# Kernel optimization log

Hardware: AMD Instinct MI355X
Metric: run time of the kernel (lower is better)

Reference implementation:

```python
import jax, jax.numpy as jnp
import numpy as np

ITERS = 4
LN_EPS = 1e-5


def build_grid(H, W):
    # standard uORF grid in [-1, 1], shape (H, W, 2), last dim = (x, y)
    x = jnp.linspace(-1.0 + 1.0 / W, 1.0 - 1.0 / W, W)
    y = jnp.linspace(-1.0 + 1.0 / H, 1.0 - 1.0 / H, H)
    yy, xx = jnp.meshgrid(y, x, indexing='ij')
    return jnp.stack([xx, yy], axis=-1)


def ln(x, g, b):
    m = jnp.mean(x, axis=-1, keepdims=True)
    v = jnp.var(x, axis=-1, keepdims=True)
    return (x - m) * jax.lax.rsqrt(v + LN_EPS) * g + b


def setup_inputs():
    key = jax.random.key(0)
    ks = jax.random.split(key, 16)
    B, H, W, C, K, Ds = 4, 64, 64, 256, 5, 256
    s = 0.02
    inp = {
        'feat': jax.random.normal(ks[0], (B, H, W, C), jnp.float32),
        'mask': (jax.random.uniform(ks[1], (K, 1, H, W)) > 0.5).astype(jnp.float32),
        'noise': jax.random.normal(ks[2], (B, K, Ds), jnp.float32),
        'slots_mu': jax.random.normal(ks[3], (1, 1, Ds), jnp.float32),
        'slots_logsigma': jax.random.normal(ks[4], (1, 1, Ds), jnp.float32) * s,
        'norm_g': jnp.ones((C,), jnp.float32), 'norm_b': jnp.zeros((C,), jnp.float32),
        'grid_W': jax.random.normal(ks[5], (C, 4), jnp.float32) * s,
        'grid_b': jnp.zeros((C,), jnp.float32),
        'k_W': jax.random.normal(ks[6], (C, C), jnp.float32) * s,
        'v_W': jax.random.normal(ks[7], (C, C), jnp.float32) * s,
        'mlp_g': jnp.ones((C,), jnp.float32), 'mlp_b': jnp.zeros((C,), jnp.float32),
        'mlp_W': jax.random.normal(ks[8], (Ds, C), jnp.float32) * s,
        'mlp_bias': jnp.zeros((Ds,), jnp.float32),
        'q_g': jnp.ones((Ds,), jnp.float32), 'q_b': jnp.zeros((Ds,), jnp.float32),
        'q_W': jax.random.normal(ks[9], (Ds, Ds), jnp.float32) * s,
        'gru_Wih': jax.random.normal(ks[10], (3 * Ds, Ds), jnp.float32) * s,
        'gru_Whh': jax.random.normal(ks[11], (3 * Ds, Ds), jnp.float32) * s,
        'gru_bih': jnp.zeros((3 * Ds,), jnp.float32),
        'gru_bhh': jnp.zeros((3 * Ds,), jnp.float32),
        'res_g': jnp.ones((Ds,), jnp.float32), 'res_b': jnp.zeros((Ds,), jnp.float32),
        'res_W': jax.random.normal(ks[12], (Ds, Ds), jnp.float32) * s,
        'res_bias': jnp.zeros((Ds,), jnp.float32),
    }
    return inp


def reference(feat, mask, noise, slots_mu, slots_logsigma, norm_g, norm_b,
              grid_W, grid_b, k_W, v_W, mlp_g, mlp_b, mlp_W, mlp_bias,
              q_g, q_b, q_W, gru_Wih, gru_Whh, gru_bih, gru_bhh,
              res_g, res_b, res_W, res_bias):
    B, H, W, C = feat.shape
    K = mask.shape[0]
    N = H * W
    Ds = slots_mu.shape[-1]
    scale = Ds ** -0.5

    grid = build_grid(H, W)                                   # (H, W, 2)
    # foreground positions: mask-weighted mean of grid -> (K, 2)
    g = jnp.transpose(grid, (2, 0, 1))[None]                  # (1, 2, H, W)
    fg_pos = jnp.sum(g * mask, axis=(2, 3)) / (jnp.sum(mask, axis=(2, 3)) + 1e-5)
    fg_pos = jnp.broadcast_to(fg_pos[None], (B, K, 2))        # (B, K, 2)

    feat_n = ln(feat.reshape(B, N, C), norm_g, norm_b)        # (B, N, C)
    mask_flat = mask.reshape(K, N)
    slot = slots_mu + jnp.exp(slots_logsigma) * noise         # (B, K, Ds)

    # k, v with relative position embedding; fg_pos never changes in-loop,
    # so compute once (the original recomputes the same values each iter).
    rel = grid.reshape(1, 1, N, 2) - fg_pos[:, :, None, :]    # (B, K, N, 2)
    rel4 = jnp.concatenate([rel, -rel], axis=-1)              # (B, K, N, 4)
    ge = rel4 @ grid_W.T + grid_b                             # (B, K, N, C)
    kbase = feat_n @ k_W.T                                    # (B, N, C)
    vbase = feat_n @ v_W.T
    kk = ln(kbase[:, None] + ge, mlp_g, mlp_b) @ mlp_W.T + mlp_bias  # (B,K,N,Ds)
    vv = ln(vbase[:, None] + ge, mlp_g, mlp_b) @ mlp_W.T + mlp_bias

    attn_vis = None
    for _ in range(ITERS):
        slot_prev = slot
        q = ln(slot, q_g, q_b) @ q_W.T                        # (B, K, Ds)
        attn = jnp.einsum('bkd,bknd->bkn', q, kk) * scale
        attn = jnp.where(mask_flat[None] == 0, -1e9, attn)
        attn = jax.nn.softmax(attn, axis=-1)                  # (B, K, N)
        upd = jnp.einsum('bkn,bknd->bkd', attn, vv)           # (B, K, Ds)
        # torch GRUCell
        x = upd.reshape(-1, Ds)
        h = slot.reshape(-1, Ds)
        gi = x @ gru_Wih.T + gru_bih
        gh = h @ gru_Whh.T + gru_bhh
        ir, iz, inn = jnp.split(gi, 3, axis=-1)
        hr, hz, hn = jnp.split(gh, 3, axis=-1)
        r = jax.nn.sigmoid(ir + hr)
        z = jax.nn.sigmoid(iz + hz)
        n = jnp.tanh(inn + r * hn)
        hnew = ((1.0 - z) * n + z * h).reshape(B, K, Ds)
        slot = (ln(hnew, res_g, res_b) @ res_W.T + res_bias) + slot_prev
        amin = attn.min(axis=-1, keepdims=True)
        amax = attn.max(axis=-1, keepdims=True)
        attn_vis = (attn - amin) / (amax - amin + 1e-5)
    return slot, fg_pos, attn_vis
```

## Files before the change

kernel.cpp:

```cpp
#include <hip/hip_runtime.h>
#include <math.h>

typedef unsigned short u16;
typedef unsigned int   u32;
typedef short bf8v __attribute__((ext_vector_type(8)));
typedef float f4v  __attribute__((ext_vector_type(4)));

static constexpr int B_=4, C_=256, K_=5, D_=256, N_=4096, IT_=4;
static constexpr float EPS_=1e-5f;
static constexpr int P0_MISC=96, P0_UQ=97, P0_FG=98, P0_GRID=103;
static constexpr int BT_QP=256, BT_TR=276, BT_GRID=404;

__device__ __forceinline__ float bf2f(u16 u){ u32 x=((u32)u)<<16; float f; __builtin_memcpy(&f,&x,4); return f; }
__device__ __forceinline__ float bflo(u32 u){ u32 x=u<<16; float f; __builtin_memcpy(&f,&x,4); return f; }
__device__ __forceinline__ float bfhi(u32 u){ u32 x=u&0xffff0000u; float f; __builtin_memcpy(&f,&x,4); return f; }
__device__ __forceinline__ u16 f2bf(float f){ u32 x; __builtin_memcpy(&x,&f,4); u32 r=x+0x7fffu+((x>>16)&1u); return (u16)(r>>16); }
__device__ __forceinline__ float ldin(const void* p, size_t i, int f){
  return f ? ((const float*)p)[i] : bf2f(((const u16*)p)[i]);
}
__device__ __forceinline__ void stout(void* p, size_t i, float v, int f){
  if (f) ((float*)p)[i]=v; else ((u16*)p)[i]=f2bf(v);
}
__device__ __forceinline__ int sw16(int row,int col){
  return row*256 + ((((col>>3)^(row&7))<<3) | (col&7));
}

__device__ __forceinline__ void breduce4(float&a,float&b,float&c,float&d,float* red){
  #pragma unroll
  for(int o=32;o>0;o>>=1){
    a+=__shfl_down(a,o,64); b+=__shfl_down(b,o,64);
    c+=__shfl_down(c,o,64); d+=__shfl_down(d,o,64);
  }
  int w=threadIdx.x>>6;
  __syncthreads();
  if((threadIdx.x&63)==0){ red[w]=a; red[4+w]=b; red[8+w]=c; red[12+w]=d; }
  __syncthreads();
  a=red[0]+red[1]+red[2]+red[3];
  b=red[4]+red[5]+red[6]+red[7];
  c=red[8]+red[9]+red[10]+red[11];
  d=red[12]+red[13]+red[14]+red[15];
}
__device__ __forceinline__ void breduce4_16(float&a,float&b,float&c,float&d,float* red){
  #pragma unroll
  for(int o=32;o>0;o>>=1){
    a+=__shfl_down(a,o,64); b+=__shfl_down(b,o,64);
    c+=__shfl_down(c,o,64); d+=__shfl_down(d,o,64);
  }
  int w=threadIdx.x>>6;
  __syncthreads();
  if((threadIdx.x&63)==0){ red[w]=a; red[16+w]=b; red[32+w]=c; red[48+w]=d; }
  __syncthreads();
  a=0;b=0;c=0;d=0;
  #pragma unroll
  for(int i=0;i<16;++i){ a+=red[i]; b+=red[16+i]; c+=red[32+i]; d+=red[48+i]; }
}

__device__ __forceinline__ int probe_f(const void* feat, float* red){
  const u32* p=(const u32*)feat;
  int t=threadIdx.x; int bad=0;
  #pragma unroll
  for(int s=0;s<8;++s){
    u32 wd=p[t+s*256];
    float lo=bf2f((u16)(wd&0xffffu));
    if(!(fabsf(lo)<1e6f)) bad++;
  }
  float bb=(float)bad, z1=0,z2=0,z3=0;
  breduce4(bb,z1,z2,z3,red);
  return (bb>=16.f)?1:0;
}

__global__ void prep0_kernel(const void* feat,
    const void* kW, const void* vW, const void* mW,
    const void* mu, const void* lsig, const void* noise,
    const void* gW, const void* gb_, const void* mg,
    const void* mb_, const void* mbias, const void* mask,
    int* flag, float* slot, float* gvec,
    u16* Wkb, u16* Wvb, u16* Wgb,
    float* Uvec, float* Qs, float* fg, void* out)
{
  __shared__ float redp[16];
  int bid=blockIdx.x;
  int t=threadIdx.x;
  int f=probe_f(feat, redp);
  if(bid==0 && t==0) *flag=f;
  __syncthreads();
  if(bid<P0_MISC){
    int which=bid>>5;
    int base=(bid&31)*2048;
    if(which==0){
      #pragma unroll
      for(int s=0;s<8;++s){ int e=base+s*256+t; Wkb[e]=f2bf(ldin(kW,e,f)); }
    } else if(which==1){
      #pragma unroll
      for(int s=0;s<8;++s){ int e=base+s*256+t; Wvb[e]=f2bf(ldin(vW,e,f)); }
    } else {
      #pragma unroll
      for(int s=0;s<8;++s){ int e=base+s*256+t; int c=e&255; Wgb[e]=f2bf(ldin(mg,c,f)*ldin(mW,e,f)); }
    }
    return;
  }
  if(bid==P0_MISC){
    #pragma unroll
    for(int s=0;s<20;++s){ int e=s*256+t; int d=e&255;
      slot[e]=ldin(mu,d,f)+expf(ldin(lsig,d,f))*ldin(noise,e,f); }
    #pragma unroll
    for(int s=0;s<3;++s){ int e=s*256+t;
      int c=e&255, sel=e>>8;
      float v;
      if(sel==0)      v=ldin(gW,c*4+0,f)-ldin(gW,c*4+2,f);
      else if(sel==1) v=ldin(gW,c*4+1,f)-ldin(gW,c*4+3,f);
      else            v=ldin(gb_,c,f);
      gvec[e]=v;
    }
    return;
  }
  __shared__ float s_a[256], s_b[256], s_c[256];
  if(bid==P0_UQ){
    __shared__ float s_mg[256], s_mb[256];
    s_a[t]=ldin(gW,t*4+0,f)-ldin(gW,t*4+2,f);
    s_b[t]=ldin(gW,t*4+1,f)-ldin(gW,t*4+3,f);
    s_c[t]=ldin(gb_,t,f);
    s_mg[t]=ldin(mg,t,f);
    s_mb[t]=ldin(mb_,t,f);
    __syncthreads();
    float u1=0,u2=0,u3=0,gw=0,bw=0;
    if(f){
      const float4* rp=(const float4*)mW + (size_t)t*64;
      #pragma unroll 8
      for(int j=0;j<64;++j){
        float4 v4=rp[j]; int c=j*4;
        float m0=v4.x,m1=v4.y,m2=v4.z,m3=v4.w;
        float w0=s_mg[c]*m0, w1=s_mg[c+1]*m1, w2=s_mg[c+2]*m2, w3=s_mg[c+3]*m3;
        u1+=s_a[c]*w0+s_a[c+1]*w1+s_a[c+2]*w2+s_a[c+3]*w3;
        u2+=s_b[c]*w0+s_b[c+1]*w1+s_b[c+2]*w2+s_b[c+3]*w3;
        u3+=s_c[c]*w0+s_c[c+1]*w1+s_c[c+2]*w2+s_c[c+3]*w3;
        gw+=w0+w1+w2+w3;
        bw+=s_mb[c]*m0+s_mb[c+1]*m1+s_mb[c+2]*m2+s_mb[c+3]*m3;
      }
    } else {
      const bf8v* rp=(const bf8v*)((const u16*)mW + (size_t)t*256);
      #pragma unroll 8
      for(int j=0;j<32;++j){
        bf8v v8=rp[j]; int c=j*8;
        #pragma unroll
        for(int e=0;e<8;++e){
          float mwv=bf2f((u16)(unsigned short)v8[e]);
          float wg=s_mg[c+e]*mwv;
          u1+=s_a[c+e]*wg; u2+=s_b[c+e]*wg; u3+=s_c[c+e]*wg; gw+=wg;
          bw+=s_mb[c+e]*mwv;
        }
      }
    }
    Uvec[t]=u1; Uvec[256+t]=u2; Uvec[512+t]=u3; Uvec[768+t]=gw;
    Uvec[1024+t]=bw+ldin(mbias,t,f);
    float a=s_a[t], b=s_b[t], cc=s_c[t];
    float s0=a*a,s1=b*b,s2=cc*cc,s3=a*b; breduce4(s0,s1,s2,s3,redp);
    float s4=a*cc,s5=b*cc,s6=a,s7=b;     breduce4(s4,s5,s6,s7,redp);
    float s8=cc,z1=0,z2=0,z3=0;          breduce4(s8,z1,z2,z3,redp);
    if(t==0){
      Qs[0]=s0; Qs[1]=s1; Qs[2]=s2; Qs[3]=s3; Qs[4]=s4; Qs[5]=s5;
      Qs[6]=s6*(1.f/256.f); Qs[7]=s7*(1.f/256.f); Qs[8]=s8*(1.f/256.f);
    }
  } else {
    int k=bid-P0_FG;
    float sx=0,sy=0,sm=0;
    #pragma unroll
    for(int s=0;s<16;++s){
      int p=t+s*256;
      float m=ldin(mask,(size_t)k*N_+p,f);
      int i=p>>6, j=p&63;
      float x=(2*j+1)*(1.0f/64.0f)-1.0f;
      float y=(2*i+1)*(1.0f/64.0f)-1.0f;
      sx+=x*m; sy+=y*m; sm+=m;
    }
    float d=0;
    breduce4(sx,sy,sm,d,redp);
    if(t==0){
      float inv=1.0f/(sm+1e-5f);
      float fx=sx*inv, fy=sy*inv;
      fg[k*2]=fx; fg[k*2+1]=fy;
      for(int b=0;b<B_;++b){
        stout(out, 5120+(b*K_+k)*2+0, fx, f);
        stout(out, 5120+(b*K_+k)*2+1, fy, f);
      }
    }
  }
}

__global__ void __launch_bounds__(512,2) base_kernel(const int* flag, const void* feat, const void* ng, const void* nb,
    const u16* Wkb, const u16* Wvb, const u16* Wgb, const float* gvec,
    float* scal, u16* PkT, u16* Pvb,
    const float* slot, const void* qg, const void* qb_, const void* qW,
    const void* rW, const void* Wih, const void* Whh,
    float* WqT, float* WrT, float* WihT, float* WhhT,
    float* qbuf)
{
  extern __shared__ u16 smem[];
  u16* bufA = smem;
  u16* bufB = smem + 16384;
  int t=threadIdx.x, f=*flag;
  if(blockIdx.x>=BT_TR){
    float (*tile)[65] = (float(*)[65])smem;
    int b2=blockIdx.x-BT_TR;
    const void* src; float* dst; int OS;
    if(b2<16){ src=qW; dst=WqT; OS=256; }
    else if(b2<32){ src=rW; dst=WrT; OS=256; b2-=16; }
    else if(b2<80){ src=Wih; dst=WihT; OS=768; b2-=32; }
    else { src=Whh; dst=WhhT; OS=768; b2-=80; }
    int r0=(b2>>2)*64, c0=(b2&3)*64;
    int lane=t&63, wv=t>>6;
    #pragma unroll
    for(int it=0;it<8;++it){
      int i=wv*8+it;
      tile[i][lane]=ldin(src,(size_t)(r0+i)*256+c0+lane,f);
    }
    __syncthreads();
    #pragma unroll
    for(int it=0;it<8;++it){
      int i=wv*8+it;
      dst[(size_t)(c0+i)*OS + r0 + lane] = tile[lane][i];
    }
    return;
  }
  if(blockIdx.x>=BT_QP){
    float* Lq =(float*)smem;
    float* pp =(float*)smem+256;
    float* red=(float*)smem+768;
    int bk=blockIdx.x-BT_QP;
    int tt=t&255, hh=t>>8, w=t>>6;
    float x=slot[bk*256+tt];
    float s=x, s2=x*x;
    #pragma unroll
    for(int o=32;o>0;o>>=1){ s+=__shfl_down(s,o,64); s2+=__shfl_down(s2,o,64); }
    if((t&63)==0){ red[w]=s; red[8+w]=s2; }
    __syncthreads();
    s=0; s2=0;
    #pragma unroll
    for(int i=0;i<8;++i){ s+=red[i]; s2+=red[8+i]; }
    float m=s*(1.f/512.f), v=s2*(1.f/512.f)-m*m;
    float lq=(x-m)*rsqrtf(v+EPS_)*ldin(qg,tt,f)+ldin(qb_,tt,f);
    if(hh==0) Lq[tt]=lq;
    __syncthreads();
    float acc=0; int cb=hh*128;
    if(f){
      const float4* rp=(const float4*)qW + ((size_t)tt*256+cb)/4;
      #pragma unroll 8
      for(int j=0;j<32;++j){
        float4 v4=rp[j]; int c=cb+j*4;
        acc+=Lq[c]*v4.x+Lq[c+1]*v4.y+Lq[c+2]*v4.z+Lq[c+3]*v4.w;
      }
    } else {
      const bf8v* rp=(const bf8v*)((const u16*)qW + (size_t)tt*256+cb);
      #pragma unroll 8
      for(int j=0;j<16;++j){
        bf8v v8=rp[j]; int c=cb+j*8;
        #pragma unroll
        for(int e=0;e<8;++e) acc+=Lq[c+e]*bf2f((u16)(unsigned short)v8[e]);
      }
    }
    pp[hh*256+tt]=acc;
    __syncthreads();
    if(hh==0) qbuf[bk*256+tt]=pp[tt]+pp[256+tt];
    return;
  }
  int w=t>>6, l=t&63;
  int quad=l>>4, m=l&15;
  int row0=blockIdx.x*64;
  {
    float g0=ldin(ng,4*l+0,f), g1=ldin(ng,4*l+1,f), g2=ldin(ng,4*l+2,f), g3=ldin(ng,4*l+3,f);
    float b0=ldin(nb,4*l+0,f), b1=ldin(nb,4*l+1,f), b2=ldin(nb,4*l+2,f), b3=ldin(nb,4*l+3,f);
    #pragma unroll
    for(int r8=0;r8<8;++r8){
      int row=8*w+r8;
      float x0,x1,x2,x3;
      if(f){
        float4 v4=((const float4*)feat)[(size_t)(row0+row)*64+l];
        x0=v4.x; x1=v4.y; x2=v4.z; x3=v4.w;
      } else {
        ushort4 uu=((const ushort4*)feat)[(size_t)(row0+row)*64+l];
        x0=bf2f(uu.x); x1=bf2f(uu.y); x2=bf2f(uu.z); x3=bf2f(uu.w);
      }
      float s=x0+x1+x2+x3, s2=x0*x0+x1*x1+x2*x2+x3*x3;
      #pragma unroll
      for(int o=32;o>0;o>>=1){ s+=__shfl_xor(s,o,64); s2+=__shfl_xor(s2,o,64); }
      float mm=s*(1.f/256.f), inv=rsqrtf(s2*(1.f/256.f)-mm*mm+EPS_);
      ushort4 o4=make_ushort4(f2bf((x0-mm)*inv*g0+b0), f2bf((x1-mm)*inv*g1+b1),
                              f2bf((x2-mm)*inv*g2+b2), f2bf((x3-mm)*inv*g3+b3));
      *(ushort4*)&bufA[sw16(row,4*l)]=o4;
    }
  }
  __syncthreads();
  {
    f4v ack[4][2], acv[4][2];
    #pragma unroll
    for(int rt=0;rt<4;++rt)
      #pragma unroll
      for(int i=0;i<2;++i){ ack[rt][i]=(f4v){0.f,0.f,0.f,0.f}; acv[rt][i]=(f4v){0.f,0.f,0.f,0.f}; }
    #pragma unroll
    for(int kk=0;kk<8;++kk){
      int kcol=kk*32+quad*8;
      bf8v af[4];
      #pragma unroll
      for(int rt=0;rt<4;++rt) af[rt]=*(bf8v*)&bufA[sw16(rt*16+m,kcol)];
      #pragma unroll
      for(int i=0;i<2;++i){
        int n=w*32+16*i+m;
        bf8v bk=*(const bf8v*)(Wkb+(size_t)n*256+kcol);
        bf8v bv=*(const bf8v*)(Wvb+(size_t)n*256+kcol);
        #pragma unroll
        for(int rt=0;rt<4;++rt){
          ack[rt][i]=__builtin_amdgcn_mfma_f32_16x16x32_bf16(af[rt],bk,ack[rt][i],0,0,0);
          acv[rt][i]=__builtin_amdgcn_mfma_f32_16x16x32_bf16(af[rt],bv,acv[rt][i],0,0,0);
        }
      }
    }
    #pragma unroll
    for(int rt=0;rt<4;++rt)
      #pragma unroll
      for(int i=0;i<2;++i){
        int n=w*32+16*i+m;
        #pragma unroll
        for(int r=0;r<4;++r)
          bufB[sw16(rt*16+quad*4+r,n)]=f2bf(ack[rt][i][r]);
      }
    __syncthreads();
    #pragma unroll
    for(int rt=0;rt<4;++rt)
      #pragma unroll
      for(int i=0;i<2;++i){
        int n=w*32+16*i+m;
        #pragma unroll
        for(int r=0;r<4;++r)
          bufA[sw16(rt*16+quad*4+r,n)]=f2bf(acv[rt][i][r]);
      }
  }
  __syncthreads();
  {
    float gA0=gvec[l], gA1=gvec[l+64], gA2=gvec[l+128], gA3=gvec[l+192];
    float gB0=gvec[256+l], gB1=gvec[256+l+64], gB2=gvec[256+l+128], gB3=gvec[256+l+192];
    float gC0=gvec[512+l], gC1=gvec[512+l+64], gC2=gvec[512+l+128], gC3=gvec[512+l+192];
    for(int r8=0;r8<8;++r8){
      int row=8*w+r8;
      float k0=bf2f(bufB[sw16(row,l)]),     k1=bf2f(bufB[sw16(row,l+64)]),
            k2=bf2f(bufB[sw16(row,l+128)]), k3=bf2f(bufB[sw16(row,l+192)]);
      float x0=bf2f(bufA[sw16(row,l)]),     x1=bf2f(bufA[sw16(row,l+64)]),
            x2=bf2f(bufA[sw16(row,l+128)]), x3=bf2f(bufA[sw16(row,l+192)]);
      float v0=k0+k1+k2+k3;
      float v1=k0*k0+k1*k1+k2*k2+k3*k3;
      float v2=k0*gA0+k1*gA1+k2*gA2+k3*gA3;
      float v3=k0*gB0+k1*gB1+k2*gB2+k3*gB3;
      float v4=k0*gC0+k1*gC1+k2*gC2+k3*gC3;
      float v5=x0+x1+x2+x3;
      float v6=x0*x0+x1*x1+x2*x2+x3*x3;
      float v7=x0*gA0+x1*gA1+x2*gA2+x3*gA3;
      float v8=x0*gB0+x1*gB1+x2*gB2+x3*gB3;
      float v9=x0*gC0+x1*gC1+x2*gC2+x3*gC3;
      #pragma unroll
      for(int o=32;o>0;o>>=1){
        v0+=__shfl_down(v0,o,64); v1+=__shfl_down(v1,o,64); v2+=__shfl_down(v2,o,64);
        v3+=__shfl_down(v3,o,64); v4+=__shfl_down(v4,o,64); v5+=__shfl_down(v5,o,64);
        v6+=__shfl_down(v6,o,64); v7+=__shfl_down(v7,o,64); v8+=__shfl_down(v8,o,64);
        v9+=__shfl_down(v9,o,64);
      }
      if(l==0){
        float* sc=scal+(size_t)(row0+row)*10;
        sc[0]=v0; sc[1]=v1; sc[2]=v2; sc[3]=v3; sc[4]=v4;
        sc[5]=v5; sc[6]=v6; sc[7]=v7; sc[8]=v8; sc[9]=v9;
      }
    }
  }
  {
    f4v apk[4][2], apv[4][2];
    #pragma unroll
    for(int rt=0;rt<4;++rt)
      #pragma unroll
      for(int i=0;i<2;++i){ apk[rt][i]=(f4v){0.f,0.f,0.f,0.f}; apv[rt][i]=(f4v){0.f,0.f,0.f,0.f}; }
    #pragma unroll
    for(int kk=0;kk<8;++kk){
      int kcol=kk*32+quad*8;
      bf8v afk[4], afv[4];
      #pragma unroll
      for(int rt=0;rt<4;++rt){
        afk[rt]=*(bf8v*)&bufB[sw16(rt*16+m,kcol)];
        afv[rt]=*(bf8v*)&bufA[sw16(rt*16+m,kcol)];
      }
      #pragma unroll
      for(int i=0;i<2;++i){
        int n=w*32+16*i+m;
        bf8v bg=*(const bf8v*)(Wgb+(size_t)n*256+kcol);
        #pragma unroll
        for(int rt=0;rt<4;++rt){
          apk[rt][i]=__builtin_amdgcn_mfma_f32_16x16x32_bf16(afk[rt],bg,apk[rt][i],0,0,0);
          apv[rt][i]=__builtin_amdgcn_mfma_f32_16x16x32_bf16(afv[rt],bg,apv[rt][i],0,0,0);
        }
      }
    }
    #pragma unroll
    for(int rt=0;rt<4;++rt)
      #pragma unroll
      for(int i=0;i<2;++i){
        int d=w*32+16*i+m;
        *(ushort4*)(PkT+(size_t)d*16384+row0+rt*16+quad*4)=
          make_ushort4(f2bf(apk[rt][i][0]),f2bf(apk[rt][i][1]),f2bf(apk[rt][i][2]),f2bf(apk[rt][i][3]));
      }
    __syncthreads();
    #pragma unroll
    for(int rt=0;rt<4;++rt)
      #pragma unroll
      for(int i=0;i<2;++i){
        int d=w*32+16*i+m;
        #pragma unroll
        for(int r=0;r<4;++r)
          bufB[sw16(rt*16+quad*4+r,d)]=f2bf(apv[rt][i][r]);
      }
  }
  __syncthreads();
  #pragma unroll
  for(int r8=0;r8<8;++r8){
    int row=8*w+r8;
    ushort4 s4=*(ushort4*)&bufB[sw16(row,4*l)];
    *(ushort4*)(Pvb+(size_t)(row0+row)*256+4*l)=s4;
  }
}

__global__ void __launch_bounds__(512) attn_kernel(const int* flag, const float* qbuf, const u16* PkT,
    const float* scal, const float* Qs, const float* Uvec, const float* fg, const void* mask,
    const u16* Pvb, float* logits, float* pmax, float* psum, float* updpart, float* sscp,
    int store_lg)
{
  __shared__ float q5[1280];
  __shared__ float un[10240];
  __shared__ float lgs[320], ivs[320], mvs[320];
  __shared__ float qs5[40], fgs[10], Qss[9], MSl[5];
  __shared__ float sred[8][5][4];
  int tid=threadIdx.x, f=*flag;
  int b=blockIdx.x>>6, ch=blockIdx.x&63;
  int w=tid>>6, l=tid&63;
  int n0=ch<<6;
  for(int p=tid;p<1280;p+=512) q5[p]=qbuf[(size_t)b*1280+p];
  if(tid<10) fgs[tid]=fg[tid];
  if(tid<9)  Qss[tid]=Qs[tid];
  __syncthreads();
  for(int p=w;p<25;p+=8){
    int k=p/5, j=p%5;
    float s=q5[k*256+l]*Uvec[j*256+l]+q5[k*256+l+64]*Uvec[j*256+l+64]
           +q5[k*256+l+128]*Uvec[j*256+l+128]+q5[k*256+l+192]*Uvec[j*256+l+192];
    #pragma unroll
    for(int o=32;o>0;o>>=1) s+=__shfl_xor(s,o,64);
    if(l==0) qs5[k*8+j]=s;
  }
  {
    int n=n0+l; size_t row=(size_t)b*N_+n;
    float dk0=0,dk1=0,dk2=0,dk3=0,dk4=0;
    int cbase=w*32;
    #pragma unroll 8
    for(int cc=0;cc<32;++cc){
      int c=cbase+cc;
      float pv=bf2f(PkT[(size_t)c*16384+row]);
      dk0+=pv*q5[c]; dk1+=pv*q5[256+c]; dk2+=pv*q5[512+c];
      dk3+=pv*q5[768+c]; dk4+=pv*q5[1024+c];
    }
    un[(w*5+0)*64+l]=dk0; un[(w*5+1)*64+l]=dk1; un[(w*5+2)*64+l]=dk2;
    un[(w*5+3)*64+l]=dk3; un[(w*5+4)*64+l]=dk4;
  }
  __syncthreads();
  if(tid<320){
    int k=tid>>6, nl=tid&63;
    float dot=0;
    #pragma unroll
    for(int j=0;j<8;++j) dot+=un[(j*5+k)*64+nl];
    int n2=n0+nl; size_t row2=(size_t)b*N_+n2;
    const float* sc=scal+row2*10;
    float rx=(2*(n2&63)+1)*(1.f/64.f)-1.f-fgs[2*k];
    float ry=(2*(n2>>6)+1)*(1.f/64.f)-1.f-fgs[2*k+1];
    float qge=rx*rx*Qss[0]+ry*ry*Qss[1]+Qss[2]+2.f*(rx*ry*Qss[3]+rx*Qss[4]+ry*Qss[5]);
    float mk=sc[0]*(1.f/256.f)+rx*Qss[6]+ry*Qss[7]+Qss[8];
    float sxk=sc[1]+2.f*(rx*sc[2]+ry*sc[3]+sc[4])+qge;
    float invK=rsqrtf(sxk*(1.f/256.f)-mk*mk+EPS_);
    float lg=invK*(dot+rx*qs5[k*8+0]+ry*qs5[k*8+1]+qs5[k*8+2]-mk*qs5[k*8+3])+qs5[k*8+4];
    float mval=ldin(mask,(size_t)k*N_+n2,f);
    lg=(mval==0.f)? -1e9f : lg*0.0625f;
    if(store_lg) logits[((size_t)(b*5+k))*N_+n2]=lg;
    lgs[tid]=lg;
    float mv=sc[5]*(1.f/256.f)+rx*Qss[6]+ry*Qss[7]+Qss[8];
    float sxv=sc[6]+2.f*(rx*sc[7]+ry*sc[8]+sc[9])+qge;
    mvs[tid]=mv;
    ivs[tid]=rsqrtf(sxv*(1.f/256.f)-mv*mv+EPS_);
  }
  __syncthreads();
  if(tid<64){
    #pragma unroll
    for(int k=0;k<5;++k){
      float v=lgs[k*64+tid];
      float M=v;
      #pragma unroll
      for(int o=32;o>0;o>>=1) M=fmaxf(M,__shfl_xor(M,o,64));
      float e=expf(v-M);
      #pragma unroll
      for(int o=32;o>0;o>>=1) e+=__shfl_xor(e,o,64);
      if(tid==0){ pmax[((size_t)(b*64+ch))*5+k]=M; psum[((size_t)(b*64+ch))*5+k]=e; MSl[k]=M; }
    }
  }
  __syncthreads();
  {
    float acc[5][4]={{0}};
    float swx[5]={0,0,0,0,0}, swy[5]={0,0,0,0,0}, sw[5]={0,0,0,0,0}, swm[5]={0,0,0,0,0};
    #pragma unroll 2
    for(int rr=0;rr<8;++rr){
      int nl=w*8+rr; int n2=n0+nl;
      size_t row=(size_t)b*N_+n2;
      uint2 pu=*(const uint2*)(Pvb+row*256+l*4);
      float px=bflo(pu.x), py=bfhi(pu.x), pz=bflo(pu.y), pw=bfhi(pu.y);
      int jx=n2&63, iy=n2>>6;
      #pragma unroll
      for(int k=0;k<5;++k){
        float wgt=expf(lgs[k*64+nl]-MSl[k])*ivs[k*64+nl];
        float rx=(2*jx+1)*(1.f/64.f)-1.f-fgs[2*k];
        float ry=(2*iy+1)*(1.f/64.f)-1.f-fgs[2*k+1];
        acc[k][0]+=wgt*px; acc[k][1]+=wgt*py; acc[k][2]+=wgt*pz; acc[k][3]+=wgt*pw;
        sw[k]+=wgt; swx[k]+=wgt*rx; swy[k]+=wgt*ry; swm[k]+=wgt*mvs[k*64+nl];
      }
    }
    #pragma unroll
    for(int k=0;k<5;++k)
      *(float4*)&un[(w*5+k)*256+l*4]=make_float4(acc[k][0],acc[k][1],acc[k][2],acc[k][3]);
    if(l==0){
      #pragma unroll
      for(int k=0;k<5;++k){ sred[w][k][0]=swx[k]; sred[w][k][1]=swy[k];
                            sred[w][k][2]=sw[k];  sred[w][k][3]=swm[k]; }
    }
  }
  __syncthreads();
  for(int p=tid;p<1280;p+=512){
    int k=p>>8, d=p&255;
    float v=0;
    #pragma unroll
    for(int j=0;j<8;++j) v+=un[(j*5+k)*256+d];
    updpart[((size_t)blockIdx.x*5+k)*256+d]=v;
  }
  if(tid<20){
    int kk=tid>>2, j=tid&3;
    float s=0;
    #pragma unroll
    for(int jj=0;jj<8;++jj) s+=sred[jj][kk][j];
    sscp[((size_t)blockIdx.x*5+kk)*4+j]=s;
  }
}

__global__ void __launch_bounds__(1024) gru_kernel(const int* flag, float* slot, const float* updpart,
    const float* sscp, const float* Uvec, const float* pmax, const float* psum, const float* logits,
    const float* WihT, const float* WhhT, const void* bih, const void* bhh,
    const void* rg, const void* rb_, const float* WrT, const void* rbias,
    const void* qg, const void* qb_, const float* WqT, float* qbuf,
    int do_vis, void* out)
{
  __shared__ float u[256], h[256], sn[256];
  __shared__ float part[4][6][256];
  __shared__ float red[64];
  __shared__ float cvec[4];
  __shared__ float fch[64];
  __shared__ float MSg[2];
  int tid=threadIdx.x, t=tid&255, g=tid>>8;
  int blk=blockIdx.x;
  int f=*flag;
  if(blk>=20){
    if(!do_vis) return;
    int bk2=blk-20, k2=bk2%K_, b2=bk2/K_;
    if(tid<64){
      float pm=pmax[((size_t)(b2*64+tid))*5+k2];
      float ps=psum[((size_t)(b2*64+tid))*5+k2];
      float M=pm;
      #pragma unroll
      for(int o=32;o>0;o>>=1) M=fmaxf(M,__shfl_xor(M,o,64));
      float e=ps*expf(pm-M);
      #pragma unroll
      for(int o=32;o>0;o>>=1) e+=__shfl_xor(e,o,64);
      if(tid==0){ MSg[0]=M; MSg[1]=1.0f/e; }
    }
    __syncthreads();
    float M=MSg[0], Sinv=MSg[1];
    float a[4]; float mn=1e30f, mx=-1e30f;
    #pragma unroll
    for(int s=0;s<4;++s){
      a[s]=expf(logits[(size_t)bk2*N_+tid+s*1024]-M)*Sinv;
      mn=fminf(mn,a[s]); mx=fmaxf(mx,a[s]);
    }
    #pragma unroll
    for(int o=32;o>0;o>>=1){ mn=fminf(mn,__shfl_down(mn,o,64)); mx=fmaxf(mx,__shfl_down(mx,o,64)); }
    int wv=tid>>6;
    __syncthreads();
    if((tid&63)==0){ red[wv]=mn; red[16+wv]=mx; }
    __syncthreads();
    mn=1e30f; mx=-1e30f;
    #pragma unroll
    for(int i=0;i<16;++i){ mn=fminf(mn,red[i]); mx=fmaxf(mx,red[16+i]); }
    float inv=1.0f/(mx-mn+1e-5f);
    #pragma unroll
    for(int s=0;s<4;++s) stout(out, 5160+(size_t)bk2*N_+tid+s*1024, (a[s]-mn)*inv, f);
    return;
  }
  int bk=blk, k=bk%K_, b=bk/K_;
  if(tid<64){
    float pm=pmax[((size_t)(b*64+tid))*5+k];
    float ps=psum[((size_t)(b*64+tid))*5+k];
    float M=pm;
    #pragma unroll
    for(int o=32;o>0;o>>=1) M=fmaxf(M,__shfl_xor(M,o,64));
    float fc=expf(pm-M);
    fch[tid]=fc;
    float e=ps*fc;
    #pragma unroll
    for(int o=32;o>0;o>>=1) e+=__shfl_xor(e,o,64);
    if(tid==0){ MSg[0]=M; MSg[1]=1.0f/e; }
  }
  __syncthreads();
  float Sinv=MSg[1];
  float ua=0;
  {
    int ch0=g*16;
    #pragma unroll 4
    for(int ci=0;ci<16;++ci){ int ch=ch0+ci; ua += fch[ch]*updpart[(((size_t)(b*64+ch))*5+k)*256+t]; }
  }
  part[g][0][t]=ua;
  if(t<4){
    float s=0;
    #pragma unroll 4
    for(int ci=0;ci<16;++ci){ int ch=g*16+ci; s += fch[ch]*sscp[(((size_t)(b*64+ch))*5+k)*4+t]; }
    part[g][1][t]=s;
  }
  __syncthreads();
  if(g==0 && t<4) cvec[t]=part[0][1][t]+part[1][1][t]+part[2][1][t]+part[3][1][t];
  __syncthreads();
  if(g==0){
    float uu=part[0][0][t]+part[1][0][t]+part[2][0][t]+part[3][0][t];
    u[t]=(uu+cvec[0]*Uvec[t]+cvec[1]*Uvec[256+t]+cvec[2]*Uvec[512+t]-cvec[3]*Uvec[768+t])*Sinv
         +Uvec[1024+t];
    h[t]=slot[bk*256+t];
  }
  __syncthreads();
  float p0=0,p1=0,p2=0,p3=0,p4=0,p5=0;
  int c0=g*64;
  #pragma unroll 8
  for(int cc=0;cc<64;++cc){
    int c=c0+cc;
    float uc=u[c], hc=h[c];
    const float* wi=WihT+(size_t)c*768+t;
    const float* wh=WhhT+(size_t)c*768+t;
    p0+=uc*wi[0]; p1+=uc*wi[256]; p2+=uc*wi[512];
    p3+=hc*wh[0]; p4+=hc*wh[256]; p5+=hc*wh[512];
  }
  part[g][0][t]=p0; part[g][1][t]=p1; part[g][2][t]=p2;
  part[g][3][t]=p3; part[g][4][t]=p4; part[g][5][t]=p5;
  __syncthreads();
  float hn=0;
  if(g==0){
    float gi0=ldin(bih,t,f)+part[0][0][t]+part[1][0][t]+part[2][0][t]+part[3][0][t];
    float gi1=ldin(bih,256+t,f)+part[0][1][t]+part[1][1][t]+part[2][1][t]+part[3][1][t];
    float gi2=ldin(bih,512+t,f)+part[0][2][t]+part[1][2][t]+part[2][2][t]+part[3][2][t];
    float gh0=ldin(bhh,t,f)+part[0][3][t]+part[1][3][t]+part[2][3][t]+part[3][3][t];
    float gh1=ldin(bhh,256+t,f)+part[0][4][t]+part[1][4][t]+part[2][4][t]+part[3][4][t];
    float gh2=ldin(bhh,512+t,f)+part[0][5][t]+part[1][5][t]+part[2][5][t]+part[3][5][t];
    float r=1.f/(1.f+expf(-(gi0+gh0)));
    float z=1.f/(1.f+expf(-(gi1+gh1)));
    float nn=tanhf(gi2+r*gh2);
    hn=(1.f-z)*nn+z*h[t];
  }
  float s=hn, sq=hn*hn, za=0, zb=0;
  breduce4_16(s,sq,za,zb,red);
  if(g==0){
    float m=s*(1.f/256.f), var=sq*(1.f/256.f)-m*m;
    u[t]=(hn-m)*rsqrtf(var+EPS_)*ldin(rg,t,f)+ldin(rb_,t,f);
  }
  __syncthreads();
  float pr=0;
  #pragma unroll 8
  for(int cc=0;cc<64;++cc){ int c=c0+cc; pr+=u[c]*WrT[(size_t)c*256+t]; }
  part[g][0][t]=pr;
  __syncthreads();
  if(g==0){
    float acc=ldin(rbias,t,f)+h[t]+part[0][0][t]+part[1][0][t]+part[2][0][t]+part[3][0][t];
    slot[bk*256+t]=acc;
    stout(out, (size_t)bk*256+t, acc, f);
    sn[t]=acc;
  }
  __syncthreads();
  float xs=(g==0)? sn[t]:0.f;
  float xq=xs*xs, zc=0, zd=0;
  breduce4_16(xs,xq,zc,zd,red);
  if(g==0){
    float m=xs*(1.f/256.f), var=xq*(1.f/256.f)-m*m;
    u[t]=(sn[t]-m)*rsqrtf(var+EPS_)*ldin(qg,t,f)+ldin(qb_,t,f);
  }
  __syncthreads();
  float pq=0;
  #pragma unroll 8
  for(int cc=0;cc<64;++cc){ int c=c0+cc; pq+=u[c]*WqT[(size_t)c*256+t]; }
  part[g][0][t]=pq;
  __syncthreads();
  if(g==0){
    float qv=part[0][0][t]+part[1][0][t]+part[2][0][t]+part[3][0][t];
    qbuf[bk*256+t]=qv;
  }
}

extern "C" void kernel_launch(void* const* d_in, const int* in_sizes, int n_in,
                              void* d_out, int out_size, void* d_ws, size_t ws_size,
                              hipStream_t stream)
{
  const void* feat =d_in[0];  const void* mask =d_in[1];  const void* noise=d_in[2];
  const void* mu   =d_in[3];  const void* lsig =d_in[4];  const void* ng   =d_in[5];
  const void* nb   =d_in[6];  const void* gW   =d_in[7];  const void* gb_  =d_in[8];
  const void* kW   =d_in[9];  const void* vW   =d_in[10]; const void* mg   =d_in[11];
  const void* mb_  =d_in[12]; const void* mW   =d_in[13]; const void* mbias=d_in[14];
  const void* qg   =d_in[15]; const void* qb_  =d_in[16]; const void* qW   =d_in[17];
  const void* Wih  =d_in[18]; const void* Whh  =d_in[19]; const void* bih  =d_in[20];
  const void* bhh  =d_in[21]; const void* rg   =d_in[22]; const void* rb_  =d_in[23];
  const void* rW   =d_in[24]; const void* rbias=d_in[25];

  char* p=(char*)d_ws;
  auto alloc=[&](size_t bytes)->char*{ char* r=p; p+=(bytes+255)&~(size_t)255; return r; };
  int*   flag   =(int*)  alloc(256);
  float* fg     =(float*)alloc(64);
  float* slot   =(float*)alloc(5120*4);
  float* qbuf   =(float*)alloc(5120*4);
  float* logits =(float*)alloc((size_t)81920*4);
  float* pmax   =(float*)alloc(1280*4);
  float* psum   =(float*)alloc(1280*4);
  float* updpart=(float*)alloc((size_t)256*5*256*4);
  float* sscp   =(float*)alloc((size_t)256*5*4*4);
  float* WqT    =(float*)alloc((size_t)65536*4);
  float* WrT    =(float*)alloc((size_t)65536*4);
  float* WihT   =(float*)alloc((size_t)196608*4);
  float* WhhT   =(float*)alloc((size_t)196608*4);
  float* gvec   =(float*)alloc(768*4);
  float* Uvec   =(float*)alloc(1280*4);
  float* Qs     =(float*)alloc(64);
  float* scal   =(float*)alloc((size_t)163840*4);
  u16*   Wkb    =(u16*)  alloc((size_t)65536*2);
  u16*   Wvb    =(u16*)  alloc((size_t)65536*2);
  u16*   Wgb    =(u16*)  alloc((size_t)65536*2);
  u16*   PkT    =(u16*)  alloc((size_t)16384*256*2);
  u16*   Pvb    =(u16*)  alloc((size_t)16384*256*2);

  prep0_kernel<<<P0_GRID,256,0,stream>>>(feat,kW,vW,mW,mu,lsig,noise,gW,gb_,mg,
                                         mb_,mbias,mask,
                                         flag,slot,gvec,Wkb,Wvb,Wgb,
                                         Uvec,Qs,fg,d_out);
  base_kernel<<<BT_GRID,512,65536,stream>>>(flag,feat,ng,nb,Wkb,Wvb,Wgb,gvec,scal,PkT,Pvb,
                                            slot,qg,qb_,qW,rW,Wih,Whh,
                                            WqT,WrT,WihT,WhhT,qbuf);
  for(int it=0; it<IT_; ++it){
    attn_kernel<<<B_*64,512,0,stream>>>(flag,qbuf,PkT,scal,Qs,Uvec,fg,mask,Pvb,
                                        logits,pmax,psum,updpart,sscp,(it==IT_-1)?1:0);
    int nb_g = (it==IT_-1)? 40 : 20;
    gru_kernel<<<nb_g,1024,0,stream>>>(flag,slot,updpart,sscp,Uvec,pmax,psum,logits,
                                       WihT,WhhT,bih,bhh,rg,rb_,WrT,rbias,
                                       qg,qb_,WqT,qbuf,(it==IT_-1)?1:0,d_out);
  }
}
```

Measured before the change: 345.8 us.

## Fuse attention and GRU per iteration using per-batch atomic grid barrier

Merges the attention and GRU kernels into one launch per iteration. Blocks bump a per-batch atomic counter after writing their partials, and designated blocks spin until all 64 blocks of that batch arrive before running the GRU or visualization step. This removes one kernel launch and its gap per iteration. The spin-wait relies on all blocks being co-resident, which risks deadlock, and the larger 1024-thread blocks leave half the threads idle during the attention phase.

```diff
diff --git a/kernel.cpp b/kernel.cpp
--- a/kernel.cpp
+++ b/kernel.cpp
@@ -74,7 +74,7 @@
     const void* mu, const void* lsig, const void* noise,
     const void* gW, const void* gb_, const void* mg,
     const void* mb_, const void* mbias, const void* mask,
-    int* flag, float* slot, float* gvec,
+    int* flag, int* cnt, float* slot, float* gvec,
     u16* Wkb, u16* Wvb, u16* Wgb,
     float* Uvec, float* Qs, float* fg, void* out)
 {
@@ -100,6 +100,7 @@
     return;
   }
   if(bid==P0_MISC){
+    if(t<16) cnt[t]=0;
     #pragma unroll
     for(int s=0;s<20;++s){ int e=s*256+t; int d=e&255;
       slot[e]=ldin(mu,d,f)+expf(ldin(lsig,d,f))*ldin(noise,e,f); }
@@ -423,33 +424,45 @@
   }
 }
 
-__global__ void __launch_bounds__(512) attn_kernel(const int* flag, const float* qbuf, const u16* PkT,
+__global__ void __launch_bounds__(1024,1) iter_kernel(
+    const int* flag, float* qbuf, const u16* PkT,
     const float* scal, const float* Qs, const float* Uvec, const float* fg, const void* mask,
     const u16* Pvb, float* logits, float* pmax, float* psum, float* updpart, float* sscp,
-    int store_lg)
+    int* cntb, int store_lg, int do_vis,
+    float* slot, const float* WihT, const float* WhhT, const void* bih, const void* bhh,
+    const void* rg, const void* rb_, const float* WrT, const void* rbias,
+    const void* qg, const void* qb_, const float* WqT, void* out)
 {
-  __shared__ float q5[1280];
-  __shared__ float un[10240];
-  __shared__ float lgs[320], ivs[320], mvs[320];
-  __shared__ float qs5[40], fgs[10], Qss[9], MSl[5];
-  __shared__ float sred[8][5][4];
+  extern __shared__ float sm[];
+  float* q5  = sm;
+  float* un  = sm+1280;
+  float* lgs = sm+11520;
+  float* ivs = sm+11840;
+  float* mvs = sm+12160;
+  float* qs5 = sm+12480;
+  float* fgs = sm+12520;
+  float* Qss = sm+12530;
+  float* MSl = sm+12539;
+  float* sredf=sm+12544;
   int tid=threadIdx.x, f=*flag;
   int b=blockIdx.x>>6, ch=blockIdx.x&63;
   int w=tid>>6, l=tid&63;
   int n0=ch<<6;
-  for(int p=tid;p<1280;p+=512) q5[p]=qbuf[(size_t)b*1280+p];
+  for(int p=tid;p<1280;p+=1024) q5[p]=qbuf[(size_t)b*1280+p];
   if(tid<10) fgs[tid]=fg[tid];
   if(tid<9)  Qss[tid]=Qs[tid];
   __syncthreads();
-  for(int p=w;p<25;p+=8){
-    int k=p/5, j=p%5;
-    float s=q5[k*256+l]*Uvec[j*256+l]+q5[k*256+l+64]*Uvec[j*256+l+64]
-           +q5[k*256+l+128]*Uvec[j*256+l+128]+q5[k*256+l+192]*Uvec[j*256+l+192];
-    #pragma unroll
-    for(int o=32;o>0;o>>=1) s+=__shfl_xor(s,o,64);
-    if(l==0) qs5[k*8+j]=s;
-  }
-  {
+  if(w<8){
+    for(int p=w;p<25;p+=8){
+      int k=p/5, j=p%5;
+      float s=q5[k*256+l]*Uvec[j*256+l]+q5[k*256+l+64]*Uvec[j*256+l+64]
+             +q5[k*256+l+128]*Uvec[j*256+l+128]+q5[k*256+l+192]*Uvec[j*256+l+192];
+      #pragma unroll
+      for(int o=32;o>0;o>>=1) s+=__shfl_xor(s,o,64);
+      if(l==0) qs5[k*8+j]=s;
+    }
+  }
+  if(tid<512){
     int n=n0+l; size_t row=(size_t)b*N_+n;
     float dk0=0,dk1=0,dk2=0,dk3=0,dk4=0;
     int cbase=w*32;
@@ -502,7 +515,7 @@
     }
   }
   __syncthreads();
-  {
+  if(tid<512){
     float acc[5][4]={{0}};
     float swx[5]={0,0,0,0,0}, swy[5]={0,0,0,0,0}, sw[5]={0,0,0,0,0}, swm[5]={0,0,0,0,0};
     #pragma unroll 2
@@ -526,12 +539,14 @@
       *(float4*)&un[(w*5+k)*256+l*4]=make_float4(acc[k][0],acc[k][1],acc[k][2],acc[k][3]);
     if(l==0){
       #pragma unroll
-      for(int k=0;k<5;++k){ sred[w][k][0]=swx[k]; sred[w][k][1]=swy[k];
-                            sred[w][k][2]=sw[k];  sred[w][k][3]=swm[k]; }
-    }
-  }
-  __syncthreads();
-  for(int p=tid;p<1280;p+=512){
+      for(int k=0;k<5;++k){
+        sredf[(w*5+k)*4+0]=swx[k]; sredf[(w*5+k)*4+1]=swy[k];
+        sredf[(w*5+k)*4+2]=sw[k];  sredf[(w*5+k)*4+3]=swm[k];
+      }
+    }
+  }
+  __syncthreads();
+  for(int p=tid;p<1280;p+=1024){
     int k=p>>8, d=p&255;
     float v=0;
     #pragma unroll
@@ -542,43 +557,42 @@
     int kk=tid>>2, j=tid&3;
     float s=0;
     #pragma unroll
-    for(int jj=0;jj<8;++jj) s+=sred[jj][kk][j];
+    for(int jj=0;jj<8;++jj) s+=sredf[(jj*5+kk)*4+j];
     sscp[((size_t)blockIdx.x*5+kk)*4+j]=s;
   }
-}
-
-__global__ void __launch_bounds__(1024) gru_kernel(const int* flag, float* slot, const float* updpart,
-    const float* sscp, const float* Uvec, const float* pmax, const float* psum, const float* logits,
-    const float* WihT, const float* WhhT, const void* bih, const void* bhh,
-    const void* rg, const void* rb_, const float* WrT, const void* rbias,
-    const void* qg, const void* qb_, const float* WqT, float* qbuf,
-    int do_vis, void* out)
-{
-  __shared__ float u[256], h[256], sn[256];
-  __shared__ float part[4][6][256];
-  __shared__ float red[64];
-  __shared__ float cvec[4];
-  __shared__ float fch[64];
-  __shared__ float MSg[2];
-  int tid=threadIdx.x, t=tid&255, g=tid>>8;
-  int blk=blockIdx.x;
-  int f=*flag;
-  if(blk>=20){
-    if(!do_vis) return;
-    int bk2=blk-20, k2=bk2%K_, b2=bk2/K_;
+  __threadfence();
+  __syncthreads();
+  if(tid==0) atomicAdd(cntb+b,1);
+  bool isgru=(ch<5);
+  bool isvis=(do_vis && ch>=8 && ch<13);
+  if(!isgru && !isvis) return;
+  if(tid==0){ while(atomicAdd(cntb+b,0)<64){} }
+  __syncthreads();
+  __threadfence();
+  float* g_u  = sm;
+  float* g_h  = sm+256;
+  float* g_sn = sm+512;
+  float* g_part=sm+768;
+  float* g_red =sm+6912;
+  float* g_cvec=sm+6976;
+  float* g_fch =sm+6980;
+  float* g_MSg =sm+7044;
+  int t=tid&255, g=tid>>8;
+  if(isvis){
+    int k2=ch-8, bk2=b*K_+k2;
     if(tid<64){
-      float pm=pmax[((size_t)(b2*64+tid))*5+k2];
-      float ps=psum[((size_t)(b2*64+tid))*5+k2];
+      float pm=pmax[((size_t)(b*64+tid))*5+k2];
+      float ps=psum[((size_t)(b*64+tid))*5+k2];
       float M=pm;
       #pragma unroll
       for(int o=32;o>0;o>>=1) M=fmaxf(M,__shfl_xor(M,o,64));
       float e=ps*expf(pm-M);
       #pragma unroll
       for(int o=32;o>0;o>>=1) e+=__shfl_xor(e,o,64);
-      if(tid==0){ MSg[0]=M; MSg[1]=1.0f/e; }
-    }
-    __syncthreads();
-    float M=MSg[0], Sinv=MSg[1];
+      if(tid==0){ g_MSg[0]=M; g_MSg[1]=1.0f/e; }
+    }
+    __syncthreads();
+    float M=g_MSg[0], Sinv=g_MSg[1];
     float a[4]; float mn=1e30f, mx=-1e30f;
     #pragma unroll
     for(int s=0;s<4;++s){
@@ -589,17 +603,17 @@
     for(int o=32;o>0;o>>=1){ mn=fminf(mn,__shfl_down(mn,o,64)); mx=fmaxf(mx,__shfl_down(mx,o,64)); }
     int wv=tid>>6;
     __syncthreads();
-    if((tid&63)==0){ red[wv]=mn; red[16+wv]=mx; }
+    if((tid&63)==0){ g_red[wv]=mn; g_red[16+wv]=mx; }
     __syncthreads();
     mn=1e30f; mx=-1e30f;
     #pragma unroll
-    for(int i=0;i<16;++i){ mn=fminf(mn,red[i]); mx=fmaxf(mx,red[16+i]); }
+    for(int i=0;i<16;++i){ mn=fminf(mn,g_red[i]); mx=fmaxf(mx,g_red[16+i]); }
     float inv=1.0f/(mx-mn+1e-5f);
     #pragma unroll
     for(int s=0;s<4;++s) stout(out, 5160+(size_t)bk2*N_+tid+s*1024, (a[s]-mn)*inv, f);
     return;
   }
-  int bk=blk, k=bk%K_, b=bk/K_;
+  int k=ch, bk=b*K_+k;
   if(tid<64){
     float pm=pmax[((size_t)(b*64+tid))*5+k];
     float ps=psum[((size_t)(b*64+tid))*5+k];
@@ -607,35 +621,35 @@
     #pragma unroll
     for(int o=32;o>0;o>>=1) M=fmaxf(M,__shfl_xor(M,o,64));
     float fc=expf(pm-M);
-    fch[tid]=fc;
+    g_fch[tid]=fc;
     float e=ps*fc;
     #pragma unroll
     for(int o=32;o>0;o>>=1) e+=__shfl_xor(e,o,64);
-    if(tid==0){ MSg[0]=M; MSg[1]=1.0f/e; }
-  }
-  __syncthreads();
-  float Sinv=MSg[1];
+    if(tid==0){ g_MSg[0]=M; g_MSg[1]=1.0f/e; }
+  }
+  __syncthreads();
+  float Sinv=g_MSg[1];
   float ua=0;
   {
     int ch0=g*16;
     #pragma unroll 4
-    for(int ci=0;ci<16;++ci){ int ch=ch0+ci; ua += fch[ch]*updpart[(((size_t)(b*64+ch))*5+k)*256+t]; }
-  }
-  part[g][0][t]=ua;
+    for(int ci=0;ci<16;++ci){ int c2=ch0+ci; ua += g_fch[c2]*updpart[(((size_t)(b*64+c2))*5+k)*256+t]; }
+  }
+  g_part[(g*6+0)*256+t]=ua;
   if(t<4){
     float s=0;
     #pragma unroll 4
-    for(int ci=0;ci<16;++ci){ int ch=g*16+ci; s += fch[ch]*sscp[(((size_t)(b*64+ch))*5+k)*4+t]; }
-    part[g][1][t]=s;
-  }
-  __syncthreads();
-  if(g==0 && t<4) cvec[t]=part[0][1][t]+part[1][1][t]+part[2][1][t]+part[3][1][t];
+    for(int ci=0;ci<16;++ci){ int c2=g*16+ci; s += g_fch[c2]*sscp[(((size_t)(b*64+c2))*5+k)*4+t]; }
+    g_part[(g*6+1)*256+t]=s;
+  }
+  __syncthreads();
+  if(g==0 && t<4) g_cvec[t]=g_part[(0*6+1)*256+t]+g_part[(1*6+1)*256+t]+g_part[(2*6+1)*256+t]+g_part[(3*6+1)*256+t];
   __syncthreads();
   if(g==0){
-    float uu=part[0][0][t]+part[1][0][t]+part[2][0][t]+part[3][0][t];
-    u[t]=(uu+cvec[0]*Uvec[t]+cvec[1]*Uvec[256+t]+cvec[2]*Uvec[512+t]-cvec[3]*Uvec[768+t])*Sinv
+    float uu=g_part[(0*6+0)*256+t]+g_part[(1*6+0)*256+t]+g_part[(2*6+0)*256+t]+g_part[(3*6+0)*256+t];
+    g_u[t]=(uu+g_cvec[0]*Uvec[t]+g_cvec[1]*Uvec[256+t]+g_cvec[2]*Uvec[512+t]-g_cvec[3]*Uvec[768+t])*Sinv
          +Uvec[1024+t];
-    h[t]=slot[bk*256+t];
+    g_h[t]=slot[bk*256+t];
   }
   __syncthreads();
   float p0=0,p1=0,p2=0,p3=0,p4=0,p5=0;
@@ -643,62 +657,62 @@
   #pragma unroll 8
   for(int cc=0;cc<64;++cc){
     int c=c0+cc;
-    float uc=u[c], hc=h[c];
+    float uc=g_u[c], hc=g_h[c];
     const float* wi=WihT+(size_t)c*768+t;
     const float* wh=WhhT+(size_t)c*768+t;
     p0+=uc*wi[0]; p1+=uc*wi[256]; p2+=uc*wi[512];
     p3+=hc*wh[0]; p4+=hc*wh[256]; p5+=hc*wh[512];
   }
-  part[g][0][t]=p0; part[g][1][t]=p1; part[g][2][t]=p2;
-  part[g][3][t]=p3; part[g][4][t]=p4; part[g][5][t]=p5;
+  g_part[(g*6+0)*256+t]=p0; g_part[(g*6+1)*256+t]=p1; g_part[(g*6+2)*256+t]=p2;
+  g_part[(g*6+3)*256+t]=p3; g_part[(g*6+4)*256+t]=p4; g_part[(g*6+5)*256+t]=p5;
   __syncthreads();
   float hn=0;
   if(g==0){
-    float gi0=ldin(bih,t,f)+part[0][0][t]+part[1][0][t]+part[2][0][t]+part[3][0][t];
-    float gi1=ldin(bih,256+t,f)+part[0][1][t]+part[1][1][t]+part[2][1][t]+part[3][1][t];
-    float gi2=ldin(bih,512+t,f)+part[0][2][t]+part[1][2][t]+part[2][2][t]+part[3][2][t];
-    float gh0=ldin(bhh,t,f)+part[0][3][t]+part[1][3][t]+part[2][3][t]+part[3][3][t];
-    float gh1=ldin(bhh,256+t,f)+part[0][4][t]+part[1][4][t]+part[2][4][t]+part[3][4][t];
-    float gh2=ldin(bhh,512+t,f)+part[0][5][t]+part[1][5][t]+part[2][5][t]+part[3][5][t];
+    float gi0=ldin(bih,t,f)+g_part[(0*6+0)*256+t]+g_part[(1*6+0)*256+t]+g_part[(2*6+0)*256+t]+g_part[(3*6+0)*256+t];
+    float gi1=ldin(bih,256+t,f)+g_part[(0*6+1)*256+t]+g_part[(1*6+1)*256+t]+g_part[(2*6+1)*256+t]+g_part[(3*6+1)*256+t];
+    float gi2=ldin(bih,512+t,f)+g_part[(0*6+2)*256+t]+g_part[(1*6+2)*256+t]+g_part[(2*6+2)*256+t]+g_part[(3*6+2)*256+t];
+    float gh0=ldin(bhh,t,f)+g_part[(0*6+3)*256+t]+g_part[(1*6+3)*256+t]+g_part[(2*6+3)*256+t]+g_part[(3*6+3)*256+t];
+    float gh1=ldin(bhh,256+t,f)+g_part[(0*6+4)*256+t]+g_part[(1*6+4)*256+t]+g_part[(2*6+4)*256+t]+g_part[(3*6+4)*256+t];
+    float gh2=ldin(bhh,512+t,f)+g_part[(0*6+5)*256+t]+g_part[(1*6+5)*256+t]+g_part[(2*6+5)*256+t]+g_part[(3*6+5)*256+t];
     float r=1.f/(1.f+expf(-(gi0+gh0)));
     float z=1.f/(1.f+expf(-(gi1+gh1)));
     float nn=tanhf(gi2+r*gh2);
-    hn=(1.f-z)*nn+z*h[t];
+    hn=(1.f-z)*nn+z*g_h[t];
   }
   float s=hn, sq=hn*hn, za=0, zb=0;
-  breduce4_16(s,sq,za,zb,red);
+  breduce4_16(s,sq,za,zb,g_red);
   if(g==0){
     float m=s*(1.f/256.f), var=sq*(1.f/256.f)-m*m;
-    u[t]=(hn-m)*rsqrtf(var+EPS_)*ldin(rg,t,f)+ldin(rb_,t,f);
+    g_u[t]=(hn-m)*rsqrtf(var+EPS_)*ldin(rg,t,f)+ldin(rb_,t,f);
   }
   __syncthreads();
   float pr=0;
   #pragma unroll 8
-  for(int cc=0;cc<64;++cc){ int c=c0+cc; pr+=u[c]*WrT[(size_t)c*256+t]; }
-  part[g][0][t]=pr;
+  for(int cc=0;cc<64;++cc){ int c=c0+cc; pr+=g_u[c]*WrT[(size_t)c*256+t]; }
+  g_part[(g*6+0)*256+t]=pr;
   __syncthreads();
   if(g==0){
-    float acc=ldin(rbias,t,f)+h[t]+part[0][0][t]+part[1][0][t]+part[2][0][t]+part[3][0][t];
+    float acc=ldin(rbias,t,f)+g_h[t]+g_part[(0*6+0)*256+t]+g_part[(1*6+0)*256+t]+g_part[(2*6+0)*256+t]+g_part[(3*6+0)*256+t];
     slot[bk*256+t]=acc;
     stout(out, (size_t)bk*256+t, acc, f);
-    sn[t]=acc;
-  }
-  __syncthreads();
-  float xs=(g==0)? sn[t]:0.f;
+    g_sn[t]=acc;
+  }
+  __syncthreads();
+  float xs=(g==0)? g_sn[t]:0.f;
   float xq=xs*xs, zc=0, zd=0;
-  breduce4_16(xs,xq,zc,zd,red);
+  breduce4_16(xs,xq,zc,zd,g_red);
   if(g==0){
     float m=xs*(1.f/256.f), var=xq*(1.f/256.f)-m*m;
-    u[t]=(sn[t]-m)*rsqrtf(var+EPS_)*ldin(qg,t,f)+ldin(qb_,t,f);
+    g_u[t]=(g_sn[t]-m)*rsqrtf(var+EPS_)*ldin(qg,t,f)+ldin(qb_,t,f);
   }
   __syncthreads();
   float pq=0;
   #pragma unroll 8
-  for(int cc=0;cc<64;++cc){ int c=c0+cc; pq+=u[c]*WqT[(size_t)c*256+t]; }
-  part[g][0][t]=pq;
+  for(int cc=0;cc<64;++cc){ int c=c0+cc; pq+=g_u[c]*WqT[(size_t)c*256+t]; }
+  g_part[(g*6+0)*256+t]=pq;
   __syncthreads();
   if(g==0){
-    float qv=part[0][0][t]+part[1][0][t]+part[2][0][t]+part[3][0][t];
+    float qv=g_part[(0*6+0)*256+t]+g_part[(1*6+0)*256+t]+g_part[(2*6+0)*256+t]+g_part[(3*6+0)*256+t];
     qbuf[bk*256+t]=qv;
   }
 }
@@ -720,6 +734,7 @@
   char* p=(char*)d_ws;
   auto alloc=[&](size_t bytes)->char*{ char* r=p; p+=(bytes+255)&~(size_t)255; return r; };
   int*   flag   =(int*)  alloc(256);
+  int*   cnt    =(int*)  alloc(64);
   float* fg     =(float*)alloc(64);
   float* slot   =(float*)alloc(5120*4);
   float* qbuf   =(float*)alloc(5120*4);
@@ -744,17 +759,17 @@
 
   prep0_kernel<<<P0_GRID,256,0,stream>>>(feat,kW,vW,mW,mu,lsig,noise,gW,gb_,mg,
                                          mb_,mbias,mask,
-                                         flag,slot,gvec,Wkb,Wvb,Wgb,
+                                         flag,cnt,slot,gvec,Wkb,Wvb,Wgb,
                                          Uvec,Qs,fg,d_out);
   base_kernel<<<BT_GRID,512,65536,stream>>>(flag,feat,ng,nb,Wkb,Wvb,Wgb,gvec,scal,PkT,Pvb,
                                             slot,qg,qb_,qW,rW,Wih,Whh,
                                             WqT,WrT,WihT,WhhT,qbuf);
   for(int it=0; it<IT_; ++it){
-    attn_kernel<<<B_*64,512,0,stream>>>(flag,qbuf,PkT,scal,Qs,Uvec,fg,mask,Pvb,
-                                        logits,pmax,psum,updpart,sscp,(it==IT_-1)?1:0);
-    int nb_g = (it==IT_-1)? 40 : 20;
-    gru_kernel<<<nb_g,1024,0,stream>>>(flag,slot,updpart,sscp,Uvec,pmax,psum,logits,
-                                       WihT,WhhT,bih,bhh,rg,rb_,WrT,rbias,
-                                       qg,qb_,WqT,qbuf,(it==IT_-1)?1:0,d_out);
-  }
-}
+    int last=(it==IT_-1)?1:0;
+    iter_kernel<<<256,1024,50816,stream>>>(flag,qbuf,PkT,scal,Qs,Uvec,fg,mask,Pvb,
+                                           logits,pmax,psum,updpart,sscp,
+                                           cnt+it*4,last,last,
+                                           slot,WihT,WhhT,bih,bhh,rg,rb_,WrT,rbias,
+                                           qg,qb_,WqT,d_out);
+  }
+}
```

After: 624.4 us. 1.81x slower.
